# Optimization experiments

Hardware: AMD Instinct MI355X
Metric: run time of the kernel (lower is better)

The kernel has to match this reference:

```python
import jax, jax.numpy as jnp
import numpy as np

N = 20000        # nodes
E = 160000       # edges
MUL = 64         # multiplicity per irrep (0e and 1o)
EDIM = 8         # scalar edge-embedding dim (radial basis)
NZ = 4           # node-attr (species one-hot) channels
AVG_NEIGH = 8.0  # avg_num_neighbors
INV_SQRT3 = float(1.0 / np.sqrt(3.0))  # CG norm for 1o x 1o -> 0e


def setup_inputs() -> dict:
    key = jax.random.key(0)
    ks = jax.random.split(key, 13)
    s = lambda fan: 1.0 / np.sqrt(fan)
    return {
        "node_feats": jax.random.normal(ks[0], (N, 256), jnp.float32),          # 64x0e | 64x1o (flattened)
        "node_attrs": jax.random.uniform(ks[1], (N, NZ), jnp.float32),
        "edge_attrs": jax.random.normal(ks[2], (E, 4), jnp.float32),            # SH lmax=1: [Y0 | Y1(3)]
        "edge_embedding": jax.random.normal(ks[3], (E, EDIM), jnp.float32),
        # linear_1 (per-irrep channel mixing)
        "W_lin1_0": jax.random.normal(ks[4], (MUL, MUL), jnp.float32),
        "W_lin1_1": jax.random.normal(ks[5], (MUL, MUL), jnp.float32),
        # radial MLP: EDIM -> EDIM -> 4*MUL tp weights
        "W_mlp1": jax.random.normal(ks[6], (EDIM, EDIM), jnp.float32),
        "W_mlp2": jax.random.normal(ks[7], (EDIM, 4 * MUL), jnp.float32),
        # linear_2: 128x0e+128x1o -> 128x0e+64x1o
        "W_lin2_0": jax.random.normal(ks[8], (2 * MUL, 2 * MUL), jnp.float32),
        "W_lin2_1": jax.random.normal(ks[9], (2 * MUL, MUL), jnp.float32),
        # self-connection FCTP weights: (u, z, w)
        "W_sc0": jax.random.normal(ks[10], (MUL, NZ, 2 * MUL), jnp.float32),
        "W_sc1": jax.random.normal(ks[11], (MUL, NZ, MUL), jnp.float32),
        "edge_index": jax.random.randint(ks[12], (2, E), 0, N, dtype=jnp.int32),
    }


def reference(node_feats, node_attrs, edge_attrs, edge_embedding,
              W_lin1_0, W_lin1_1, W_mlp1, W_mlp2,
              W_lin2_0, W_lin2_1, W_sc0, W_sc1, edge_index):
    edge_src, edge_dst = edge_index[0], edge_index[1]

    # split node feats into irrep blocks: 64x0e scalars, 64x1o vectors
    x0 = node_feats[:, :MUL]                         # [N, 64]
    x1 = node_feats[:, MUL:].reshape(N, MUL, 3)      # [N, 64, 3]

    # linear_1 (e3nn Linear, per-irrep, 1/sqrt(fan_in))
    inv = 1.0 / np.sqrt(MUL)
    h0 = (x0 @ W_lin1_0) * inv                       # [N, 64]
    h1 = jnp.einsum("nud,uv->nvd", x1, W_lin1_1) * inv

    # radial MLP -> per-edge UVU weights (e3nn FullyConnectedNet: no bias, silu, 1/sqrt(fan_in))
    inv_e = 1.0 / np.sqrt(EDIM)
    hid = jax.nn.silu((edge_embedding @ W_mlp1) * inv_e)
    w = (hid @ W_mlp2) * inv_e                       # [E, 4*MUL]
    w1, w2, w3, w4 = w[:, :MUL], w[:, MUL:2*MUL], w[:, 2*MUL:3*MUL], w[:, 3*MUL:]

    # gather source-node features per edge
    g0 = h0[edge_src]                                # [E, 64]
    g1 = h1[edge_src]                                # [E, 64, 3]
    a0 = edge_attrs[:, :1]                           # [E, 1]  Y0
    a1 = edge_attrs[:, 1:]                           # [E, 3]  Y1

    # UVU tensor product paths (v = 1 for SH attrs)
    m0_a = w1 * g0 * a0                              # 0e x 0e -> 0e
    m0_b = w4 * jnp.einsum("eud,ed->eu", g1, a1) * INV_SQRT3   # 1o x 1o -> 0e
    m1_a = (w2 * g0)[:, :, None] * a1[:, None, :]    # 0e x 1o -> 1o
    m1_b = (w3[:, :, None] * g1) * a0[:, :, None]    # 1o x 0e -> 1o
    msg0 = jnp.concatenate([m0_a, m0_b], axis=1)     # [E, 128]
    msg1 = jnp.concatenate([m1_a, m1_b], axis=1)     # [E, 128, 3]

    # scatter_add to destination nodes, normalize by sqrt(avg_num_neighbors)
    inv_n = 1.0 / np.sqrt(AVG_NEIGH)
    s0 = jax.ops.segment_sum(msg0, edge_dst, num_segments=N) * inv_n   # [N, 128]
    s1 = jax.ops.segment_sum(msg1, edge_dst, num_segments=N) * inv_n   # [N, 128, 3]

    # linear_2: 128x0e+128x1o -> 128x0e (64 scalars + 64 gates) + 64x1o
    inv2 = 1.0 / np.sqrt(2 * MUL)
    u0 = (s0 @ W_lin2_0) * inv2                      # [N, 128]
    u1 = jnp.einsum("nud,uw->nwd", s1, W_lin2_1) * inv2   # [N, 64, 3]

    # self-connection FCTP with 0e node attrs (species-conditioned linear)
    inv_sc = 1.0 / np.sqrt(MUL * NZ)
    sc0 = jnp.einsum("nu,nz,uzw->nw", x0, node_attrs, W_sc0) * inv_sc
    sc1 = jnp.einsum("nud,nz,uzw->nwd", x1, node_attrs, W_sc1) * inv_sc
    t0 = u0 + sc0                                    # [N, 128]
    t1 = u1 + sc1                                    # [N, 64, 3]

    # Gate nonlinearity: silu on scalars, silu(gates) * vectors
    scalars = jax.nn.silu(t0[:, :MUL])               # [N, 64]
    gates = jax.nn.silu(t0[:, MUL:])                 # [N, 64]
    vectors = gates[:, :, None] * t1                 # [N, 64, 3]

    out = jnp.concatenate([scalars, vectors.reshape(N, MUL * 3)], axis=1)  # [N, 256]
    # resnet (irreps match input)
    return node_feats + out
```

## Files before the change

kernel.cpp:

```cpp
#include <hip/hip_runtime.h>
#include <hip/hip_bf16.h>
#include <math.h>

#define N 20000
#define E 160000
#define MUL 64
#define EDIM 8
#define NZ 4

#define INV_SQRT_MUL 0.125f
#define INV_E 0.35355339059327373f
#define INV_N 0.35355339059327373f
#define INV2 0.08838834764831845f
#define INV_SC 0.0625f
#define INV_SQRT3 0.5773502691896258f

typedef unsigned short u16;
typedef unsigned int u32;
typedef short bf16x8 __attribute__((ext_vector_type(8)));
typedef float f32x4 __attribute__((ext_vector_type(4)));

__device__ __forceinline__ float silu(float v) {
    return v / (1.0f + __expf(-v));
}
__device__ __forceinline__ u16 f2bf(float f) {
    union { float f; unsigned int u; } v; v.f = f;
    unsigned int r = (v.u + 0x7FFFu + ((v.u >> 16) & 1u)) >> 16;
    return (u16)r;
}
__device__ __forceinline__ float bflo(u32 p) {
    union { unsigned int u; float f; } v; v.u = p << 16; return v.f;
}
__device__ __forceinline__ float bfhi(u32 p) {
    union { unsigned int u; float f; } v; v.u = p & 0xFFFF0000u; return v.f;
}
#define MFMA(a, b, c) __builtin_amdgcn_mfma_f32_16x16x32_bf16(a, b, c, 0, 0, 0)

__device__ __forceinline__ void gll16(const u16* g, u16* l) {
    __builtin_amdgcn_global_load_lds(
        (const __attribute__((address_space(1))) u32*)g,
        (__attribute__((address_space(3))) u32*)l, 16, 0, 0);
}


#define PREP_B  1250
#define WCONV_B 288
#define HID_B   5000
#define LIST_B  625

__global__ __launch_bounds__(256) void k_front(
    const float* __restrict__ x,
    const float* __restrict__ eemb, const int* __restrict__ eidx,
    const float* __restrict__ W20, const float* __restrict__ Wsc0,
    const float* __restrict__ W21, const float* __restrict__ Wsc1,
    const float* __restrict__ W0, const float* __restrict__ W1,
    const float* __restrict__ Wm1,
    u16* __restrict__ A1, u16* __restrict__ x1p,
    u16* __restrict__ Bt1m, u16* __restrict__ Bt1z, u16* __restrict__ Bt2,
    u16* __restrict__ hc, float* __restrict__ hid,
    int* __restrict__ head, int2* __restrict__ nl)
{
    const int b = blockIdx.x;
    const int tid = threadIdx.x;

    if (b < PREP_B) {
        __shared__ float xr[16][256];
        __shared__ u16 sxb0[16 * 68];
        __shared__ u16 sxb1[48 * 68];
        const int n0 = b * 16;
        const int lane = tid & 63, wave = tid >> 6;
        const int quad = lane >> 4, l16 = lane & 15;

        const float* Wsrc = (wave == 0) ? W0 : W1;
        bf16x8 bw[4][2];
        #pragma unroll
        for (int ct = 0; ct < 4; ++ct)
            #pragma unroll
            for (int kk = 0; kk < 2; ++kk)
                #pragma unroll
                for (int j = 0; j < 8; ++j)
                    bw[ct][kk][j] = (short)f2bf(
                        Wsrc[(kk * 32 + quad * 8 + j) * 64 + ct * 16 + l16]
                        * INV_SQRT_MUL);

        #pragma unroll
        for (int t = 0; t < 16; ++t)
            xr[t][tid] = x[(size_t)(n0 + t) * 256 + tid];
        __syncthreads();

        #pragma unroll
        for (int i = 0; i < 4; ++i) {
            const int idx = tid * 4 + i;
            const int row = idx >> 6, col = idx & 63;
            const u16 v = f2bf(xr[row][col]);
            sxb0[row * 68 + col] = v;
            A1[(size_t)(n0 + row) * 192 + 128 + col] = v;
        }
        #pragma unroll
        for (int i = 0; i < 12; ++i) {
            const int idx = tid * 12 + i;
            const int lrow = idx >> 6, u = idx & 63;
            const int t = (lrow * 21846) >> 16;
            const int d = lrow - t * 3;
            const u16 v = f2bf(xr[t][64 + u * 3 + d]);
            sxb1[lrow * 68 + u] = v;
            x1p[((size_t)(3 * n0) + lrow) * 64 + u] = v;
        }
        __syncthreads();

        f32x4 acc[4] = {};
        if (wave == 0) {
            #pragma unroll
            for (int kk = 0; kk < 2; ++kk) {
                bf16x8 a = *(const bf16x8*)(sxb0 + l16 * 68 + kk * 32 + quad * 8);
                #pragma unroll
                for (int ct = 0; ct < 4; ++ct)
                    acc[ct] = MFMA(a, bw[ct][kk], acc[ct]);
            }
            #pragma unroll
            for (int ct = 0; ct < 4; ++ct)
                #pragma unroll
                for (int r = 0; r < 4; ++r) {
                    const int row = n0 + quad * 4 + r;
                    const int vv = ct * 16 + l16;
                    hc[(size_t)row * 256 + vv * 4] = f2bf(acc[ct][r]);
                }
        } else {
            const int rt = wave - 1;
            #pragma unroll
            for (int kk = 0; kk < 2; ++kk) {
                bf16x8 a = *(const bf16x8*)(sxb1 + (rt * 16 + l16) * 68 + kk * 32 + quad * 8);
                #pragma unroll
                for (int ct = 0; ct < 4; ++ct)
                    acc[ct] = MFMA(a, bw[ct][kk], acc[ct]);
            }
            #pragma unroll
            for (int ct = 0; ct < 4; ++ct)
                #pragma unroll
                for (int r = 0; r < 4; ++r) {
                    const int lrow = rt * 16 + quad * 4 + r;
                    const int t = (lrow * 21846) >> 16;
                    const int d = lrow - t * 3;
                    const int vv = ct * 16 + l16;
                    hc[(size_t)(n0 + t) * 256 + vv * 4 + 1 + d] = f2bf(acc[ct][r]);
                }
        }
    } else if (b < PREP_B + WCONV_B) {
        const int i = (b - PREP_B) * 256 + tid;
        if (i < 16384) {
            int w = i >> 7, k = i & 127;
            Bt1m[i] = f2bf(W20[k * 128 + w]);
        } else if (i < 49152) {
            int j = i - 16384;
            int z = j >> 13, r = j & 8191, w = r >> 6, k = r & 63;
            Bt1z[j] = f2bf(Wsc0[(k * 4 + z) * 128 + w] * INV_SC);
        } else {
            int j = i - 49152;
            int w = j / 384, k = j % 384;
            float v = (k < 128) ? W21[k * 64 + w] : Wsc1[(k - 128) * 64 + w];
            Bt2[j] = f2bf(v);
        }
    } else if (b < PREP_B + WCONV_B + HID_B) {
        const int i = (b - PREP_B - WCONV_B) * 256 + tid;
        const int e = i >> 3, k = i & 7;
        float s = 0.f;
        #pragma unroll
        for (int j = 0; j < 8; ++j)
            s += eemb[(size_t)e * 8 + j] * Wm1[j * 8 + k];
        hid[i] = silu(s * INV_E);
    } else {
        const int e = (b - PREP_B - WCONV_B - HID_B) * 256 + tid;
        if (e < E) {
            int src = eidx[e];
            int dst = eidx[E + e];
            int old = atomicExch(&head[dst], e);
            nl[e] = make_int2(old, src);
        }
    }
}

__global__ __launch_bounds__(256) void k_gather(
    const int* __restrict__ head, const int2* __restrict__ nl,
    const float* __restrict__ eattr, const float* __restrict__ hid,
    const u32* __restrict__ hc2, const float* __restrict__ Wm2,
    u16* __restrict__ A1, u16* __restrict__ A2g)
{
    const int lane = threadIdx.x & 63;
    const int n = blockIdx.x * 4 + (threadIdx.x >> 6);

    float wm0[8], wm1[8], wm2r[8], wm3[8];
    #pragma unroll
    for (int k = 0; k < 8; ++k) {
        wm0[k]  = Wm2[k * 256 + lane];
        wm1[k]  = Wm2[k * 256 + 64 + lane];
        wm2r[k] = Wm2[k * 256 + 128 + lane];
        wm3[k]  = Wm2[k * 256 + 192 + lane];
    }

    float acc0a = 0.f, acc0b = 0.f;
    float s1a[3] = {0.f, 0.f, 0.f}, s1b[3] = {0.f, 0.f, 0.f};

    int e0 = head[n];
    if (e0 != -1) {
        int2 v0 = nl[e0];
        float4 ea = ((const float4*)eattr)[e0];
        float4 hA = ((const float4*)hid)[(size_t)e0 * 2];
        float4 hB = ((const float4*)hid)[(size_t)e0 * 2 + 1];
        uint2  hp = ((const uint2*)hc2)[(size_t)v0.y * 64 + lane];
        int e1 = v0.x;
        int2 v1 = make_int2(-1, 0);
        if (e1 != -1) v1 = nl[e1];

        while (true) {
            int e2 = -1;
            int2 v2 = make_int2(-1, 0);
            float4 eaN, hAN, hBN; uint2 hpN;
            if (e1 != -1) {
                e2 = v1.x;
                if (e2 != -1) v2 = nl[e2];
                eaN = ((const float4*)eattr)[e1];
                hAN = ((const float4*)hid)[(size_t)e1 * 2];
                hBN = ((const float4*)hid)[(size_t)e1 * 2 + 1];
                hpN = ((const uint2*)hc2)[(size_t)v1.y * 64 + lane];
            }

            float w1 = hA.x*wm0[0]+hA.y*wm0[1]+hA.z*wm0[2]+hA.w*wm0[3]
                     + hB.x*wm0[4]+hB.y*wm0[5]+hB.z*wm0[6]+hB.w*wm0[7];
            float w2 = hA.x*wm1[0]+hA.y*wm1[1]+hA.z*wm1[2]+hA.w*wm1[3]
                     + hB.x*wm1[4]+hB.y*wm1[5]+hB.z*wm1[6]+hB.w*wm1[7];
            float w3 = hA.x*wm2r[0]+hA.y*wm2r[1]+hA.z*wm2r[2]+hA.w*wm2r[3]
                     + hB.x*wm2r[4]+hB.y*wm2r[5]+hB.z*wm2r[6]+hB.w*wm2r[7];
            float w4 = hA.x*wm3[0]+hA.y*wm3[1]+hA.z*wm3[2]+hA.w*wm3[3]
                     + hB.x*wm3[4]+hB.y*wm3[5]+hB.z*wm3[6]+hB.w*wm3[7];
            const float g0 = bflo(hp.x), g1x = bfhi(hp.x);
            const float g1y = bflo(hp.y), g1z = bfhi(hp.y);
            acc0a += w1 * g0 * ea.x;
            acc0b += w4 * (g1x * ea.y + g1y * ea.z + g1z * ea.w);
            const float wg = w2 * g0, w3a = w3 * ea.x;
            s1a[0] += wg * ea.y;  s1a[1] += wg * ea.z;  s1a[2] += wg * ea.w;
            s1b[0] += w3a * g1x;  s1b[1] += w3a * g1y;  s1b[2] += w3a * g1z;

            if (e1 == -1) break;
            ea = eaN; hA = hAN; hB = hBN; hp = hpN;
            e1 = e2; v1 = v2;
        }
    }

    const float f = INV_E * INV_N * INV2;
    u16* a1p = &A1[(size_t)n * 192];
    a1p[lane]      = f2bf(acc0a * f);
    a1p[64 + lane] = f2bf(acc0b * f * INV_SQRT3);
    #pragma unroll
    for (int d = 0; d < 3; ++d) {
        u16* a2p = &A2g[((size_t)n * 3 + d) * 128];
        a2p[lane]      = f2bf(s1a[d] * f);
        a2p[64 + lane] = f2bf(s1b[d] * f);
    }
}

__global__ __launch_bounds__(512, 4) void k_gemm_fused(
    const u16* __restrict__ A1, const u16* __restrict__ A2g,
    const u16* __restrict__ x1p,
    const u16* __restrict__ Bt1m, const u16* __restrict__ Bt1z,
    const u16* __restrict__ Bt2,
    const float* __restrict__ attrs, const float* __restrict__ x,
    float* __restrict__ out)
{
    const int lane = threadIdx.x & 63;
    const int wave = threadIdx.x >> 6;
    const int quad = lane >> 4, l16 = lane & 15;
    const int n0 = blockIdx.x * 16;
    const float4* at4 = (const float4*)attrs;

    __shared__ __align__(16) u16 sA1[16 * 192];
    __shared__ __align__(16) u16 sA2[48 * 128];
    __shared__ float st0[16][132];
    __shared__ float st1[48][68];

    {
        const u16* gA1 = A1 + (size_t)n0 * 192;
        const u16* gA2 = A2g + (size_t)(3 * n0) * 128;
        #pragma unroll
        for (int i = 0; i < 3; ++i) {
            const int cc = wave + i * 8;
            if (cc < 6) {
                const int Lu = cc * 512 + lane * 8;
                const int row = Lu / 192;
                const int src = Lu ^ ((row & 7) << 3);
                gll16(gA1 + src, &sA1[cc * 512]);
            } else if (cc < 18) {
                const int Lu = (cc - 6) * 512 + lane * 8;
                const int row = Lu >> 7;
                const int src = Lu ^ ((row & 7) << 3);
                gll16(gA2 + src, &sA2[(cc - 6) * 512]);
            }
        }
    }

    const u16 *bz0p = nullptr, *bz1p = nullptr;
    bf16x8 PB[8], PC[8];
    u32 XQ[3][8];
    float4 atv[3];

    if (wave < 4) {
        const u16* b0p = Bt1m + (size_t)(wave * 16 + l16) * 128 + quad * 8;
        const u16* b1p = Bt1m + (size_t)((wave + 4) * 16 + l16) * 128 + quad * 8;
        bz0p = Bt1z + (size_t)(wave * 16 + l16) * 64 + quad * 8;
        bz1p = Bt1z + (size_t)((wave + 4) * 16 + l16) * 64 + quad * 8;
        #pragma unroll
        for (int kt = 0; kt < 4; ++kt) {
            PB[kt]     = *(const bf16x8*)(b0p + kt * 32);
            PB[4 + kt] = *(const bf16x8*)(b1p + kt * 32);
        }
        #pragma unroll
        for (int z = 0; z < 2; ++z)
            #pragma unroll
            for (int kt = 0; kt < 2; ++kt) {
                PC[z * 2 + kt]     = *(const bf16x8*)(bz0p + z * 8192 + kt * 32);
                PC[4 + z * 2 + kt] = *(const bf16x8*)(bz1p + z * 8192 + kt * 32);
            }
    } else {
        const int ct = wave - 4;
        const u16* b2p = Bt2 + (size_t)(ct * 16 + l16) * 384 + quad * 8;
        const u16* xq0 = x1p + (size_t)(3 * n0 + l16) * 64 + quad * 2;
        #pragma unroll
        for (int kt = 0; kt < 4; ++kt)
            PB[kt] = *(const bf16x8*)(b2p + kt * 32);
        #pragma unroll
        for (int kt = 0; kt < 8; ++kt) {
            bf16x8 v = *(const bf16x8*)(b2p + 128 + kt * 32);
            if (kt < 4) PB[4 + kt] = v; else PC[kt - 4] = v;
        }
        #pragma unroll
        for (int rt = 0; rt < 3; ++rt)
            #pragma unroll
            for (int kt = 0; kt < 8; ++kt)
                XQ[rt][kt] = *(const u32*)(xq0 + rt * 16 * 64 + kt * 8);
        #pragma unroll
        for (int rt = 0; rt < 3; ++rt) {
            const int ro = rt * 16 + l16;
            const int nn = (ro * 21846) >> 16;
            const float4 v = at4[n0 + nn];
            atv[rt].x = v.x * INV_SC; atv[rt].y = v.y * INV_SC;
            atv[rt].z = v.z * INV_SC; atv[rt].w = v.w * INV_SC;
        }
    }

    const int c = threadIdx.x & 255;
    const int th = threadIdx.x >> 8;
    float xv[8];
    #pragma unroll
    for (int i = 0; i < 8; ++i)
        xv[i] = x[(size_t)(n0 + i * 2 + th) * 256 + c];

    __syncthreads();

    if (wave < 4) {
        f32x4 m0 = {}, m1 = {};
        #pragma unroll
        for (int kt = 0; kt < 4; ++kt) {
            const int off = l16 * 192 + kt * 32 + quad * 8;
            bf16x8 a0 = *(const bf16x8*)(sA1 + (off ^ ((l16 & 7) << 3)));
            m0 = MFMA(a0, PB[kt], m0);
            m1 = MFMA(a0, PB[4 + kt], m1);
        }
        bf16x8 a0s[2];
        #pragma unroll
        for (int kt = 0; kt < 2; ++kt) {
            const int off = l16 * 192 + 128 + kt * 32 + quad * 8;
            a0s[kt] = *(const bf16x8*)(sA1 + (off ^ ((l16 & 7) << 3)));
        }
        f32x4 z0[4] = {}, z1[4] = {};
        #pragma unroll
        for (int z = 0; z < 2; ++z)
            #pragma unroll
            for (int kt = 0; kt < 2; ++kt) {
                z0[z] = MFMA(a0s[kt], PC[z * 2 + kt], z0[z]);
                z1[z] = MFMA(a0s[kt], PC[4 + z * 2 + kt], z1[z]);
            }
        #pragma unroll
        for (int z = 0; z < 2; ++z)
            #pragma unroll
            for (int kt = 0; kt < 2; ++kt) {
                bf16x8 d0 = *(const bf16x8*)(bz0p + (z + 2) * 8192 + kt * 32);
                bf16x8 d1 = *(const bf16x8*)(bz1p + (z + 2) * 8192 + kt * 32);
                z0[z + 2] = MFMA(a0s[kt], d0, z0[z + 2]);
                z1[z + 2] = MFMA(a0s[kt], d1, z1[z + 2]);
            }

        #pragma unroll
        for (int r = 0; r < 4; ++r) {
            const int r0 = quad * 4 + r;
            const float4 a = at4[n0 + r0];
            st0[r0][wave * 16 + l16] =
                m0[r] + a.x * z0[0][r] + a.y * z0[1][r] + a.z * z0[2][r] + a.w * z0[3][r];
            st0[r0][(wave + 4) * 16 + l16] =
                m1[r] + a.x * z1[0][r] + a.y * z1[1][r] + a.z * z1[2][r] + a.w * z1[3][r];
        }
    } else {
        const int ct = wave - 4;
        f32x4 mt[3] = {};
        #pragma unroll
        for (int kt = 0; kt < 4; ++kt) {
            #pragma unroll
            for (int rt = 0; rt < 3; ++rt) {
                const int row = rt * 16 + l16;
                const int off = row * 128 + kt * 32 + quad * 8;
                bf16x8 a = *(const bf16x8*)(sA2 + (off ^ ((row & 7) << 3)));
                mt[rt] = MFMA(a, PB[kt], mt[rt]);
            }
        }
        #pragma unroll
        for (int kt = 0; kt < 8; ++kt) {
            const bf16x8 b2 = (kt < 4) ? PB[4 + kt] : PC[kt - 4];
            #pragma unroll
            for (int rt = 0; rt < 3; ++rt) {
                const u32 xp = XQ[rt][kt];
                const float xa = bflo(xp), xb = bfhi(xp);
                bf16x8 af;
                af[0] = (short)f2bf(xa * atv[rt].x); af[1] = (short)f2bf(xa * atv[rt].y);
                af[2] = (short)f2bf(xa * atv[rt].z); af[3] = (short)f2bf(xa * atv[rt].w);
                af[4] = (short)f2bf(xb * atv[rt].x); af[5] = (short)f2bf(xb * atv[rt].y);
                af[6] = (short)f2bf(xb * atv[rt].z); af[7] = (short)f2bf(xb * atv[rt].w);
                mt[rt] = MFMA(af, b2, mt[rt]);
            }
        }

        #pragma unroll
        for (int r = 0; r < 4; ++r) {
            const int r0 = quad * 4 + r;
            st1[r0][ct * 16 + l16]      = mt[0][r];
            st1[16 + r0][ct * 16 + l16] = mt[1][r];
            st1[32 + r0][ct * 16 + l16] = mt[2][r];
        }
    }

    __syncthreads();

    #pragma unroll
    for (int i = 0; i < 8; ++i) {
        const int t = i * 2 + th;
        float o;
        if (c < 64) {
            o = xv[i] + silu(st0[t][c]);
        } else {
            int r = c - 64;
            int w = (r * 21846) >> 16;
            int d = r - w * 3;
            o = xv[i] + silu(st0[t][64 + w]) * st1[t * 3 + d][w];
        }
        out[(size_t)(n0 + t) * 256 + c] = o;
    }
}

extern "C" void kernel_launch(void* const* d_in, const int* in_sizes, int n_in,
                              void* d_out, int out_size, void* d_ws, size_t ws_size,
                              hipStream_t stream) {
    const float* node_feats = (const float*)d_in[0];
    const float* node_attrs = (const float*)d_in[1];
    const float* edge_attrs = (const float*)d_in[2];
    const float* edge_emb   = (const float*)d_in[3];
    const float* W_lin1_0   = (const float*)d_in[4];
    const float* W_lin1_1   = (const float*)d_in[5];
    const float* W_mlp1     = (const float*)d_in[6];
    const float* W_mlp2     = (const float*)d_in[7];
    const float* W_lin2_0   = (const float*)d_in[8];
    const float* W_lin2_1   = (const float*)d_in[9];
    const float* W_sc0      = (const float*)d_in[10];
    const float* W_sc1      = (const float*)d_in[11];
    const int*   edge_index = (const int*)d_in[12];
    float* out = (float*)d_out;

    char* p = (char*)d_ws;
    float* hid = (float*)p;                 p += (size_t)E * 8 * 4;
    u16* hc    = (u16*)p;                   p += (size_t)N * 256 * 2;
    u16* A1    = (u16*)p;                   p += (size_t)N * 192 * 2;
    u16* A2g   = (u16*)p;                   p += (size_t)N * 3 * 128 * 2;
    u16* x1p   = (u16*)p;                   p += (size_t)N * 3 * 64 * 2;
    u16* Bt1m  = (u16*)p;                   p += 16384 * 2;
    u16* Bt1z  = (u16*)p;                   p += 32768 * 2;
    u16* Bt2   = (u16*)p;                   p += 24576 * 2;
    int* head  = (int*)p;                   p += N * 4;
    int2* nl   = (int2*)p;                  p += (size_t)E * 8;

    hipMemsetAsync(head, 0xFF, N * sizeof(int), stream);

    k_front<<<PREP_B + WCONV_B + HID_B + LIST_B, 256, 0, stream>>>(
        node_feats, edge_emb, edge_index,
        W_lin2_0, W_sc0, W_lin2_1, W_sc1, W_lin1_0, W_lin1_1, W_mlp1,
        A1, x1p, Bt1m, Bt1z, Bt2, hc, hid, head, nl);
    k_gather<<<N / 4, 256, 0, stream>>>(head, nl, edge_attrs, hid,
                                        (const u32*)hc, W_mlp2, A1, A2g);
    k_gemm_fused<<<1250, 512, 0, stream>>>(A1, A2g, x1p, Bt1m, Bt1z, Bt2,
                                           node_attrs, node_feats, out);
}
```

Baseline: 201.5 us.

## Fuse edge gather into the GEMM kernel, keeping aggregated features in LDS

The separate gather kernel is merged into the final GEMM kernel. Each wave walks the linked edge lists for two nodes at once, interleaving the two chains, and writes the aggregated scalar and vector sums straight into swizzled shared memory, so the A1/A2g global intermediates and one kernel launch go away. The x0 bf16 operand is now converted from node_feats inside the GEMM, and the B-operand weights are loaded just before use instead of being prefetched into registers. The cost is that the latency-bound gather now runs at the GEMM kernel's occupancy (512 threads, 8 waves per block covering 16 nodes), and load imbalance between the two interleaved lists can stall the whole block at the barrier.

```diff
diff --git a/kernel.cpp b/kernel.cpp
--- a/kernel.cpp
+++ b/kernel.cpp
@@ -35,12 +35,6 @@
     union { unsigned int u; float f; } v; v.u = p & 0xFFFF0000u; return v.f;
 }
 #define MFMA(a, b, c) __builtin_amdgcn_mfma_f32_16x16x32_bf16(a, b, c, 0, 0, 0)
-
-__device__ __forceinline__ void gll16(const u16* g, u16* l) {
-    __builtin_amdgcn_global_load_lds(
-        (const __attribute__((address_space(1))) u32*)g,
-        (__attribute__((address_space(3))) u32*)l, 16, 0, 0);
-}
 
 
 #define PREP_B  1250
@@ -55,7 +49,7 @@
     const float* __restrict__ W21, const float* __restrict__ Wsc1,
     const float* __restrict__ W0, const float* __restrict__ W1,
     const float* __restrict__ Wm1,
-    u16* __restrict__ A1, u16* __restrict__ x1p,
+    u16* __restrict__ x1p,
     u16* __restrict__ Bt1m, u16* __restrict__ Bt1z, u16* __restrict__ Bt2,
     u16* __restrict__ hc, float* __restrict__ hid,
     int* __restrict__ head, int2* __restrict__ nl)
@@ -92,9 +86,7 @@
         for (int i = 0; i < 4; ++i) {
             const int idx = tid * 4 + i;
             const int row = idx >> 6, col = idx & 63;
-            const u16 v = f2bf(xr[row][col]);
-            sxb0[row * 68 + col] = v;
-            A1[(size_t)(n0 + row) * 192 + 128 + col] = v;
+            sxb0[row * 68 + col] = f2bf(xr[row][col]);
         }
         #pragma unroll
         for (int i = 0; i < 12; ++i) {
@@ -179,87 +171,10 @@
     }
 }
 
-__global__ __launch_bounds__(256) void k_gather(
+__global__ __launch_bounds__(512, 4) void k_gf(
     const int* __restrict__ head, const int2* __restrict__ nl,
     const float* __restrict__ eattr, const float* __restrict__ hid,
     const u32* __restrict__ hc2, const float* __restrict__ Wm2,
-    u16* __restrict__ A1, u16* __restrict__ A2g)
-{
-    const int lane = threadIdx.x & 63;
-    const int n = blockIdx.x * 4 + (threadIdx.x >> 6);
-
-    float wm0[8], wm1[8], wm2r[8], wm3[8];
-    #pragma unroll
-    for (int k = 0; k < 8; ++k) {
-        wm0[k]  = Wm2[k * 256 + lane];
-        wm1[k]  = Wm2[k * 256 + 64 + lane];
-        wm2r[k] = Wm2[k * 256 + 128 + lane];
-        wm3[k]  = Wm2[k * 256 + 192 + lane];
-    }
-
-    float acc0a = 0.f, acc0b = 0.f;
-    float s1a[3] = {0.f, 0.f, 0.f}, s1b[3] = {0.f, 0.f, 0.f};
-
-    int e0 = head[n];
-    if (e0 != -1) {
-        int2 v0 = nl[e0];
-        float4 ea = ((const float4*)eattr)[e0];
-        float4 hA = ((const float4*)hid)[(size_t)e0 * 2];
-        float4 hB = ((const float4*)hid)[(size_t)e0 * 2 + 1];
-        uint2  hp = ((const uint2*)hc2)[(size_t)v0.y * 64 + lane];
-        int e1 = v0.x;
-        int2 v1 = make_int2(-1, 0);
-        if (e1 != -1) v1 = nl[e1];
-
-        while (true) {
-            int e2 = -1;
-            int2 v2 = make_int2(-1, 0);
-            float4 eaN, hAN, hBN; uint2 hpN;
-            if (e1 != -1) {
-                e2 = v1.x;
-                if (e2 != -1) v2 = nl[e2];
-                eaN = ((const float4*)eattr)[e1];
-                hAN = ((const float4*)hid)[(size_t)e1 * 2];
-                hBN = ((const float4*)hid)[(size_t)e1 * 2 + 1];
-                hpN = ((const uint2*)hc2)[(size_t)v1.y * 64 + lane];
-            }
-
-            float w1 = hA.x*wm0[0]+hA.y*wm0[1]+hA.z*wm0[2]+hA.w*wm0[3]
-                     + hB.x*wm0[4]+hB.y*wm0[5]+hB.z*wm0[6]+hB.w*wm0[7];
-            float w2 = hA.x*wm1[0]+hA.y*wm1[1]+hA.z*wm1[2]+hA.w*wm1[3]
-                     + hB.x*wm1[4]+hB.y*wm1[5]+hB.z*wm1[6]+hB.w*wm1[7];
-            float w3 = hA.x*wm2r[0]+hA.y*wm2r[1]+hA.z*wm2r[2]+hA.w*wm2r[3]
-                     + hB.x*wm2r[4]+hB.y*wm2r[5]+hB.z*wm2r[6]+hB.w*wm2r[7];
-            float w4 = hA.x*wm3[0]+hA.y*wm3[1]+hA.z*wm3[2]+hA.w*wm3[3]
-                     + hB.x*wm3[4]+hB.y*wm3[5]+hB.z*wm3[6]+hB.w*wm3[7];
-            const float g0 = bflo(hp.x), g1x = bfhi(hp.x);
-            const float g1y = bflo(hp.y), g1z = bfhi(hp.y);
-            acc0a += w1 * g0 * ea.x;
-            acc0b += w4 * (g1x * ea.y + g1y * ea.z + g1z * ea.w);
-            const float wg = w2 * g0, w3a = w3 * ea.x;
-            s1a[0] += wg * ea.y;  s1a[1] += wg * ea.z;  s1a[2] += wg * ea.w;
-            s1b[0] += w3a * g1x;  s1b[1] += w3a * g1y;  s1b[2] += w3a * g1z;
-
-            if (e1 == -1) break;
-            ea = eaN; hA = hAN; hB = hBN; hp = hpN;
-            e1 = e2; v1 = v2;
-        }
-    }
-
-    const float f = INV_E * INV_N * INV2;
-    u16* a1p = &A1[(size_t)n * 192];
-    a1p[lane]      = f2bf(acc0a * f);
-    a1p[64 + lane] = f2bf(acc0b * f * INV_SQRT3);
-    #pragma unroll
-    for (int d = 0; d < 3; ++d) {
-        u16* a2p = &A2g[((size_t)n * 3 + d) * 128];
-        a2p[lane]      = f2bf(s1a[d] * f);
-        a2p[64 + lane] = f2bf(s1b[d] * f);
-    }
-}
-
-__global__ __launch_bounds__(512, 4) void k_gemm_fused(
-    const u16* __restrict__ A1, const u16* __restrict__ A2g,
     const u16* __restrict__ x1p,
     const u16* __restrict__ Bt1m, const u16* __restrict__ Bt1z,
     const u16* __restrict__ Bt2,
@@ -272,79 +187,114 @@
     const int n0 = blockIdx.x * 16;
     const float4* at4 = (const float4*)attrs;
 
-    __shared__ __align__(16) u16 sA1[16 * 192];
-    __shared__ __align__(16) u16 sA2[48 * 128];
+    __shared__ u16 sA1[16 * 128];
+    __shared__ u16 sA2[48 * 128];
     __shared__ float st0[16][132];
     __shared__ float st1[48][68];
 
+    float wm0[8], wm1[8], wm2r[8], wm3[8];
+    #pragma unroll
+    for (int k = 0; k < 8; ++k) {
+        wm0[k]  = Wm2[k * 256 + lane];
+        wm1[k]  = Wm2[k * 256 + 64 + lane];
+        wm2r[k] = Wm2[k * 256 + 128 + lane];
+        wm3[k]  = Wm2[k * 256 + 192 + lane];
+    }
+
+    auto edgeC = [&](const float4& ea, const float4& hA, const float4& hB,
+                     const uint2& hp, float& a0, float& a3,
+                     float* s1a, float* s1b) {
+        float w1 = hA.x*wm0[0]+hA.y*wm0[1]+hA.z*wm0[2]+hA.w*wm0[3]
+                 + hB.x*wm0[4]+hB.y*wm0[5]+hB.z*wm0[6]+hB.w*wm0[7];
+        float w2 = hA.x*wm1[0]+hA.y*wm1[1]+hA.z*wm1[2]+hA.w*wm1[3]
+                 + hB.x*wm1[4]+hB.y*wm1[5]+hB.z*wm1[6]+hB.w*wm1[7];
+        float w3 = hA.x*wm2r[0]+hA.y*wm2r[1]+hA.z*wm2r[2]+hA.w*wm2r[3]
+                 + hB.x*wm2r[4]+hB.y*wm2r[5]+hB.z*wm2r[6]+hB.w*wm2r[7];
+        float w4 = hA.x*wm3[0]+hA.y*wm3[1]+hA.z*wm3[2]+hA.w*wm3[3]
+                 + hB.x*wm3[4]+hB.y*wm3[5]+hB.z*wm3[6]+hB.w*wm3[7];
+        const float g0 = bflo(hp.x), g1x = bfhi(hp.x);
+        const float g1y = bflo(hp.y), g1z = bfhi(hp.y);
+        a0 += w1 * g0 * ea.x;
+        a3 += w4 * (g1x * ea.y + g1y * ea.z + g1z * ea.w);
+        const float wg = w2 * g0, w3a = w3 * ea.x;
+        s1a[0] += wg * ea.y;  s1a[1] += wg * ea.z;  s1a[2] += wg * ea.w;
+        s1b[0] += w3a * g1x;  s1b[1] += w3a * g1y;  s1b[2] += w3a * g1z;
+    };
+
+    const int nA = n0 + 2 * wave;
+    float aA0 = 0.f, aA3 = 0.f, sAa[3] = {0,0,0}, sAb[3] = {0,0,0};
+    float aB0 = 0.f, aB3 = 0.f, sBa[3] = {0,0,0}, sBb[3] = {0,0,0};
+
+    int eA = head[nA];
+    int eB = head[nA + 1];
+    int2 vA = make_int2(-1, 0), vB = make_int2(-1, 0);
+    float4 eaA, hAA, hBA; uint2 hpA;
+    float4 eaB, hAB, hBB; uint2 hpB;
+    if (eA != -1) {
+        vA  = nl[eA];
+        eaA = ((const float4*)eattr)[eA];
+        hAA = ((const float4*)hid)[(size_t)eA * 2];
+        hBA = ((const float4*)hid)[(size_t)eA * 2 + 1];
+        hpA = ((const uint2*)hc2)[(size_t)vA.y * 64 + lane];
+    }
+    if (eB != -1) {
+        vB  = nl[eB];
+        eaB = ((const float4*)eattr)[eB];
+        hAB = ((const float4*)hid)[(size_t)eB * 2];
+        hBB = ((const float4*)hid)[(size_t)eB * 2 + 1];
+        hpB = ((const uint2*)hc2)[(size_t)vB.y * 64 + lane];
+    }
+
+    while (eA != -1 || eB != -1) {
+        int enA = -1, enB = -1;
+        int2 vnA = make_int2(-1, 0), vnB = make_int2(-1, 0);
+        float4 eaNA, hANA, hBNA; uint2 hpNA;
+        float4 eaNB, hANB, hBNB; uint2 hpNB;
+        if (eA != -1) {
+            enA = vA.x;
+            if (enA != -1) {
+                vnA  = nl[enA];
+                eaNA = ((const float4*)eattr)[enA];
+                hANA = ((const float4*)hid)[(size_t)enA * 2];
+                hBNA = ((const float4*)hid)[(size_t)enA * 2 + 1];
+                hpNA = ((const uint2*)hc2)[(size_t)vnA.y * 64 + lane];
+            }
+        }
+        if (eB != -1) {
+            enB = vB.x;
+            if (enB != -1) {
+                vnB  = nl[enB];
+                eaNB = ((const float4*)eattr)[enB];
+                hANB = ((const float4*)hid)[(size_t)enB * 2];
+                hBNB = ((const float4*)hid)[(size_t)enB * 2 + 1];
+                hpNB = ((const uint2*)hc2)[(size_t)vnB.y * 64 + lane];
+            }
+        }
+
+        if (eA != -1) edgeC(eaA, hAA, hBA, hpA, aA0, aA3, sAa, sAb);
+        if (eB != -1) edgeC(eaB, hAB, hBB, hpB, aB0, aB3, sBa, sBb);
+
+        if (eA != -1) { eA = enA; vA = vnA; eaA = eaNA; hAA = hANA; hBA = hBNA; hpA = hpNA; }
+        if (eB != -1) { eB = enB; vB = vnB; eaB = eaNB; hAB = hANB; hBB = hBNB; hpB = hpNB; }
+    }
+
     {
-        const u16* gA1 = A1 + (size_t)n0 * 192;
-        const u16* gA2 = A2g + (size_t)(3 * n0) * 128;
-        #pragma unroll
-        for (int i = 0; i < 3; ++i) {
-            const int cc = wave + i * 8;
-            if (cc < 6) {
-                const int Lu = cc * 512 + lane * 8;
-                const int row = Lu / 192;
-                const int src = Lu ^ ((row & 7) << 3);
-                gll16(gA1 + src, &sA1[cc * 512]);
-            } else if (cc < 18) {
-                const int Lu = (cc - 6) * 512 + lane * 8;
-                const int row = Lu >> 7;
-                const int src = Lu ^ ((row & 7) << 3);
-                gll16(gA2 + src, &sA2[(cc - 6) * 512]);
-            }
-        }
-    }
-
-    const u16 *bz0p = nullptr, *bz1p = nullptr;
-    bf16x8 PB[8], PC[8];
-    u32 XQ[3][8];
-    float4 atv[3];
-
-    if (wave < 4) {
-        const u16* b0p = Bt1m + (size_t)(wave * 16 + l16) * 128 + quad * 8;
-        const u16* b1p = Bt1m + (size_t)((wave + 4) * 16 + l16) * 128 + quad * 8;
-        bz0p = Bt1z + (size_t)(wave * 16 + l16) * 64 + quad * 8;
-        bz1p = Bt1z + (size_t)((wave + 4) * 16 + l16) * 64 + quad * 8;
-        #pragma unroll
-        for (int kt = 0; kt < 4; ++kt) {
-            PB[kt]     = *(const bf16x8*)(b0p + kt * 32);
-            PB[4 + kt] = *(const bf16x8*)(b1p + kt * 32);
-        }
-        #pragma unroll
-        for (int z = 0; z < 2; ++z)
-            #pragma unroll
-            for (int kt = 0; kt < 2; ++kt) {
-                PC[z * 2 + kt]     = *(const bf16x8*)(bz0p + z * 8192 + kt * 32);
-                PC[4 + z * 2 + kt] = *(const bf16x8*)(bz1p + z * 8192 + kt * 32);
-            }
-    } else {
-        const int ct = wave - 4;
-        const u16* b2p = Bt2 + (size_t)(ct * 16 + l16) * 384 + quad * 8;
-        const u16* xq0 = x1p + (size_t)(3 * n0 + l16) * 64 + quad * 2;
-        #pragma unroll
-        for (int kt = 0; kt < 4; ++kt)
-            PB[kt] = *(const bf16x8*)(b2p + kt * 32);
-        #pragma unroll
-        for (int kt = 0; kt < 8; ++kt) {
-            bf16x8 v = *(const bf16x8*)(b2p + 128 + kt * 32);
-            if (kt < 4) PB[4 + kt] = v; else PC[kt - 4] = v;
-        }
-        #pragma unroll
-        for (int rt = 0; rt < 3; ++rt)
-            #pragma unroll
-            for (int kt = 0; kt < 8; ++kt)
-                XQ[rt][kt] = *(const u32*)(xq0 + rt * 16 * 64 + kt * 8);
-        #pragma unroll
-        for (int rt = 0; rt < 3; ++rt) {
-            const int ro = rt * 16 + l16;
-            const int nn = (ro * 21846) >> 16;
-            const float4 v = at4[n0 + nn];
-            atv[rt].x = v.x * INV_SC; atv[rt].y = v.y * INV_SC;
-            atv[rt].z = v.z * INV_SC; atv[rt].w = v.w * INV_SC;
-        }
-    }
+        const float f = INV_E * INV_N * INV2;
+        const int rrA = 2 * wave, rrB = 2 * wave + 1;
+        sA1[rrA * 128 + (lane ^ ((rrA & 7) << 3))]        = f2bf(aA0 * f);
+        sA1[rrA * 128 + ((64 + lane) ^ ((rrA & 7) << 3))] = f2bf(aA3 * f * INV_SQRT3);
+        sA1[rrB * 128 + (lane ^ ((rrB & 7) << 3))]        = f2bf(aB0 * f);
+        sA1[rrB * 128 + ((64 + lane) ^ ((rrB & 7) << 3))] = f2bf(aB3 * f * INV_SQRT3);
+        #pragma unroll
+        for (int d = 0; d < 3; ++d) {
+            const int lrA = rrA * 3 + d, lrB = rrB * 3 + d;
+            sA2[lrA * 128 + (lane ^ ((lrA & 7) << 3))]        = f2bf(sAa[d] * f);
+            sA2[lrA * 128 + ((64 + lane) ^ ((lrA & 7) << 3))] = f2bf(sAb[d] * f);
+            sA2[lrB * 128 + (lane ^ ((lrB & 7) << 3))]        = f2bf(sBa[d] * f);
+            sA2[lrB * 128 + ((64 + lane) ^ ((lrB & 7) << 3))] = f2bf(sBb[d] * f);
+        }
+    }
+    __syncthreads();
 
     const int c = threadIdx.x & 255;
     const int th = threadIdx.x >> 8;
@@ -353,39 +303,43 @@
     for (int i = 0; i < 8; ++i)
         xv[i] = x[(size_t)(n0 + i * 2 + th) * 256 + c];
 
-    __syncthreads();
-
     if (wave < 4) {
+        const u16* b0p  = Bt1m + (size_t)(wave * 16 + l16) * 128 + quad * 8;
+        const u16* b1p  = Bt1m + (size_t)((wave + 4) * 16 + l16) * 128 + quad * 8;
+        const u16* bz0p = Bt1z + (size_t)(wave * 16 + l16) * 64 + quad * 8;
+        const u16* bz1p = Bt1z + (size_t)((wave + 4) * 16 + l16) * 64 + quad * 8;
+
+        bf16x8 a0s[2];
+        #pragma unroll
+        for (int kt = 0; kt < 2; ++kt) {
+            const float* xp = x + (size_t)(n0 + l16) * 256 + kt * 32 + quad * 8;
+            const float4 xa = *(const float4*)xp;
+            const float4 xb = *(const float4*)(xp + 4);
+            a0s[kt][0] = (short)f2bf(xa.x); a0s[kt][1] = (short)f2bf(xa.y);
+            a0s[kt][2] = (short)f2bf(xa.z); a0s[kt][3] = (short)f2bf(xa.w);
+            a0s[kt][4] = (short)f2bf(xb.x); a0s[kt][5] = (short)f2bf(xb.y);
+            a0s[kt][6] = (short)f2bf(xb.z); a0s[kt][7] = (short)f2bf(xb.w);
+        }
+
         f32x4 m0 = {}, m1 = {};
         #pragma unroll
         for (int kt = 0; kt < 4; ++kt) {
-            const int off = l16 * 192 + kt * 32 + quad * 8;
+            const int off = l16 * 128 + kt * 32 + quad * 8;
             bf16x8 a0 = *(const bf16x8*)(sA1 + (off ^ ((l16 & 7) << 3)));
-            m0 = MFMA(a0, PB[kt], m0);
-            m1 = MFMA(a0, PB[4 + kt], m1);
-        }
-        bf16x8 a0s[2];
-        #pragma unroll
-        for (int kt = 0; kt < 2; ++kt) {
-            const int off = l16 * 192 + 128 + kt * 32 + quad * 8;
-            a0s[kt] = *(const bf16x8*)(sA1 + (off ^ ((l16 & 7) << 3)));
+            bf16x8 b0 = *(const bf16x8*)(b0p + kt * 32);
+            bf16x8 b1 = *(const bf16x8*)(b1p + kt * 32);
+            m0 = MFMA(a0, b0, m0);
+            m1 = MFMA(a0, b1, m1);
         }
         f32x4 z0[4] = {}, z1[4] = {};
         #pragma unroll
-        for (int z = 0; z < 2; ++z)
+        for (int z = 0; z < 4; ++z)
             #pragma unroll
             for (int kt = 0; kt < 2; ++kt) {
-                z0[z] = MFMA(a0s[kt], PC[z * 2 + kt], z0[z]);
-                z1[z] = MFMA(a0s[kt], PC[4 + z * 2 + kt], z1[z]);
-            }
-        #pragma unroll
-        for (int z = 0; z < 2; ++z)
-            #pragma unroll
-            for (int kt = 0; kt < 2; ++kt) {
-                bf16x8 d0 = *(const bf16x8*)(bz0p + (z + 2) * 8192 + kt * 32);
-                bf16x8 d1 = *(const bf16x8*)(bz1p + (z + 2) * 8192 + kt * 32);
-                z0[z + 2] = MFMA(a0s[kt], d0, z0[z + 2]);
-                z1[z + 2] = MFMA(a0s[kt], d1, z1[z + 2]);
+                bf16x8 c0 = *(const bf16x8*)(bz0p + z * 8192 + kt * 32);
+                bf16x8 c1 = *(const bf16x8*)(bz1p + z * 8192 + kt * 32);
+                z0[z] = MFMA(a0s[kt], c0, z0[z]);
+                z1[z] = MFMA(a0s[kt], c1, z1[z]);
             }
 
         #pragma unroll
@@ -399,20 +353,40 @@
         }
     } else {
         const int ct = wave - 4;
+        const u16* b2p = Bt2 + (size_t)(ct * 16 + l16) * 384 + quad * 8;
+        const u16* xq0 = x1p + (size_t)(3 * n0 + l16) * 64 + quad * 2;
+
+        u32 XQ[3][8];
+        #pragma unroll
+        for (int rt = 0; rt < 3; ++rt)
+            #pragma unroll
+            for (int kt = 0; kt < 8; ++kt)
+                XQ[rt][kt] = *(const u32*)(xq0 + rt * 16 * 64 + kt * 8);
+        float4 atv[3];
+        #pragma unroll
+        for (int rt = 0; rt < 3; ++rt) {
+            const int ro = rt * 16 + l16;
+            const int nn = (ro * 21846) >> 16;
+            const float4 v = at4[n0 + nn];
+            atv[rt].x = v.x * INV_SC; atv[rt].y = v.y * INV_SC;
+            atv[rt].z = v.z * INV_SC; atv[rt].w = v.w * INV_SC;
+        }
+
         f32x4 mt[3] = {};
         #pragma unroll
         for (int kt = 0; kt < 4; ++kt) {
+            bf16x8 b2 = *(const bf16x8*)(b2p + kt * 32);
             #pragma unroll
             for (int rt = 0; rt < 3; ++rt) {
                 const int row = rt * 16 + l16;
                 const int off = row * 128 + kt * 32 + quad * 8;
                 bf16x8 a = *(const bf16x8*)(sA2 + (off ^ ((row & 7) << 3)));
-                mt[rt] = MFMA(a, PB[kt], mt[rt]);
+                mt[rt] = MFMA(a, b2, mt[rt]);
             }
         }
         #pragma unroll
         for (int kt = 0; kt < 8; ++kt) {
-            const bf16x8 b2 = (kt < 4) ? PB[4 + kt] : PC[kt - 4];
+            bf16x8 b2 = *(const bf16x8*)(b2p + 128 + kt * 32);
             #pragma unroll
             for (int rt = 0; rt < 3; ++rt) {
                 const u32 xp = XQ[rt][kt];
@@ -474,8 +448,6 @@
     char* p = (char*)d_ws;
     float* hid = (float*)p;                 p += (size_t)E * 8 * 4;
     u16* hc    = (u16*)p;                   p += (size_t)N * 256 * 2;
-    u16* A1    = (u16*)p;                   p += (size_t)N * 192 * 2;
-    u16* A2g   = (u16*)p;                   p += (size_t)N * 3 * 128 * 2;
     u16* x1p   = (u16*)p;                   p += (size_t)N * 3 * 64 * 2;
     u16* Bt1m  = (u16*)p;                   p += 16384 * 2;
     u16* Bt1z  = (u16*)p;                   p += 32768 * 2;
@@ -488,9 +460,9 @@
     k_front<<<PREP_B + WCONV_B + HID_B + LIST_B, 256, 0, stream>>>(
         node_feats, edge_emb, edge_index,
         W_lin2_0, W_sc0, W_lin2_1, W_sc1, W_lin1_0, W_lin1_1, W_mlp1,
-        A1, x1p, Bt1m, Bt1z, Bt2, hc, hid, head, nl);
-    k_gather<<<N / 4, 256, 0, stream>>>(head, nl, edge_attrs, hid,
-                                        (const u32*)hc, W_mlp2, A1, A2g);
-    k_gemm_fused<<<1250, 512, 0, stream>>>(A1, A2g, x1p, Bt1m, Bt1z, Bt2,
-                                           node_attrs, node_feats, out);
-}
+        x1p, Bt1m, Bt1z, Bt2, hc, hid, head, nl);
+    k_gf<<<1250, 512, 0, stream>>>(head, nl, edge_attrs, hid,
+                                   (const u32*)hc, W_mlp2, x1p,
+                                   Bt1m, Bt1z, Bt2,
+                                   node_attrs, node_feats, out);
+}
```

After: 217.3 us. +7.9%, slower.
